# Performance work log

Measured on AMD Instinct MI355X. Metric: run time of the kernel, lower is better.

## Reference

```python
import jax, jax.numpy as jnp
import numpy as np

B, S, L, K, E, V = 2048, 4, 16, 8, 256, 128  # batch, max_steps, tokens/step, landmarks/cell, emb_sz, vocab


def setup_inputs() -> dict:
    key = jax.random.key(0)
    ks = jax.random.split(key, 10)
    std = 1.0 / (E * 9)
    return {
        "gold_table": jax.random.normal(ks[0], (11, E), jnp.float32),
        "map_table": jax.random.normal(ks[1], (V, E), jnp.float32) * 0.01,  # init_std=0.01
        "conv_weight": jax.random.uniform(ks[2], (E, E, 3, 3), jnp.float32, -std, std),
        "action_table": jax.random.normal(ks[3], (4, 32), jnp.float32),
        "action_W": jax.random.normal(ks[4], (9, 32), jnp.float32) * (1.0 / np.sqrt(32.0)),
        "action_b": jnp.zeros((9,), jnp.float32),
        "goldstandard": jax.random.randint(ks[5], (B, S, L), 0, 11),
        "actions": jax.random.randint(ks[6], (B, S - 1), 0, 4),
        "landmarks": jax.random.randint(ks[7], (B, 4, 4, K), 0, V),
        "y": jax.random.randint(ks[8], (B, 2), 0, 4),
    }


def _extract_patches(x):
    # x: [B,E,4,4] -> [B,9,E,16]; 3x3 neighborhoods with zero padding (conv padding=1)
    xp = jnp.pad(x, ((0, 0), (0, 0), (1, 1), (1, 1)))
    shifts = [xp[:, :, dh:dh + 4, dw:dw + 4].reshape(x.shape[0], x.shape[1], 16)
              for dh in range(3) for dw in range(3)]
    return jnp.stack(shifts, axis=1)


def reference(gold_table, map_table, conv_weight, action_table, action_W, action_b,
              goldstandard, actions, landmarks, y):
    Bn = y.shape[0]
    # goldstandard features: per-step embed+sum over tokens, concat over steps -> [B, S*E]
    emb = gold_table[goldstandard].sum(axis=2).reshape(Bn, -1)
    # MapEmbedding2d with padding_idx=0: zero row 0, embed, sum over landmark list
    mt = map_table.at[0].set(0.0)
    l_emb = mt[landmarks].sum(axis=3).transpose(0, 3, 1, 2)  # [B,E,4,4]
    # action-conditioned 3x3 masks, one per action
    action_out = action_table @ action_W.T + action_b  # [4,9]
    masks = jax.nn.softmax(action_out, axis=1)  # [4,9]
    Wr = conv_weight.reshape(E, E, 9)  # [O,I,tap]
    l_embs = [l_emb]
    cur = l_emb
    for j in range(S - 1):
        # per-sample routed mask == dispatch-to-expert conv; fused gather+masked-conv+scatter
        m = masks[actions[:, j]]  # [B,9]
        patches = _extract_patches(cur)  # [B,9,E,16]
        out = jnp.einsum('btip,bt,oit->bop', patches, m, Wr).reshape(Bn, E, 4, 4)
        l_embs.append(out)
        cur = out
    lm = jnp.concatenate(l_embs, axis=1).reshape(Bn, S * E, 16)  # [B, S*E, 16]
    logits = jnp.einsum('bcp,bc->bp', lm, emb)  # bmm(landmarks^T, emb)
    prob = jax.nn.softmax(logits, axis=1)
    y_true = y[:, 0] * 4 + y[:, 1]
    # torch CrossEntropyLoss applied to prob (softmax twice, as in the original)
    logp = jax.nn.log_softmax(prob, axis=1)
    loss = -jnp.take_along_axis(logp, y_true[:, None], axis=1).mean()
    acc = (jnp.argmax(prob, axis=1) == y_true).astype(jnp.float32).mean()
    return loss, acc, prob
```

## Files before the change

### kernel.cpp

```cpp
#include <hip/hip_runtime.h>
#include <hip/hip_bf16.h>

typedef __attribute__((ext_vector_type(4))) float f32x4;
typedef __attribute__((ext_vector_type(8))) short short8;

__device__ __forceinline__ float bf2f(ushort u) {
    union { unsigned int u; float f; } x; x.u = ((unsigned int)u) << 16; return x.f;
}
__device__ __forceinline__ ushort f2bf(float f) {
    union { float f; unsigned int u; } x; x.f = f;
    unsigned int u = x.u;
    unsigned int r = (u + 0x7fffu + ((u >> 16) & 1u)) >> 16;
    return (ushort)r;
}
__device__ __forceinline__ void gload16(const ushort* g, ushort* l) {
    __builtin_amdgcn_global_load_lds(
        (const __attribute__((address_space(1))) unsigned int*)g,
        (__attribute__((address_space(3))) unsigned int*)l, 16, 0, 0);
}

__global__ __launch_bounds__(256) void k_wfold(
    const float* __restrict__ conv_w, const float* __restrict__ a_table,
    const float* __restrict__ a_W, const float* __restrict__ a_b,
    ushort* __restrict__ Wa)
{
    __shared__ float ao[4][9];
    __shared__ float m[4][9];
    const int o = blockIdx.x, tid = threadIdx.x;
    if (tid < 36) {
        const int a = tid / 9, t = tid % 9;
        float s = a_b[t];
        for (int c = 0; c < 32; c++) s += a_table[a * 32 + c] * a_W[t * 32 + c];
        ao[a][t] = s;
    }
    __syncthreads();
    if (tid < 4) {
        float mx = -1e30f;
        for (int t = 0; t < 9; t++) mx = fmaxf(mx, ao[tid][t]);
        float e[9], z = 0.f;
        for (int t = 0; t < 9; t++) { e[t] = expf(ao[tid][t] - mx); z += e[t]; }
        for (int t = 0; t < 9; t++) m[tid][t] = e[t] / z;
    }
    __syncthreads();
    float w9[9];
    #pragma unroll
    for (int t = 0; t < 9; t++) w9[t] = conv_w[(o * 256 + tid) * 9 + t];
    #pragma unroll
    for (int a = 0; a < 4; a++)
        #pragma unroll
        for (int t = 0; t < 9; t++)
            Wa[(size_t)((a << 8) + o) * 2304 + t * 256 + tid] = f2bf(m[a][t] * w9[t]);
}

__global__ __launch_bounds__(256) void k_bucket(
    const int* __restrict__ actions, int* __restrict__ cnt, int* __restrict__ list)
{
    const int idx = blockIdx.x * 256 + threadIdx.x;
    const int j = idx >> 11, b = idx & 2047;
    const int a = actions[b * 3 + j];
    const int pos = atomicAdd(&cnt[j * 4 + a], 1);
    list[((j * 4 + a) << 11) + pos] = b;
}

__global__ __launch_bounds__(256) void k_lemb(
    const float* __restrict__ mapt, const int* __restrict__ lms,
    ushort* __restrict__ c0)
{
    const int b = blockIdx.x, e = threadIdx.x;
    for (int p = 0; p < 16; p++) {
        const int* lm = lms + (b * 16 + p) * 8;
        float s = 0.f;
        #pragma unroll
        for (int k = 0; k < 8; k++) {
            const int idx = lm[k];
            if (idx) s += mapt[idx * 256 + e];
        }
        c0[(size_t)(b * 16 + p) * 256 + e] = f2bf(s);
    }
}

__global__ __launch_bounds__(256, 2) void k_conv(
    const ushort* __restrict__ cur, const ushort* __restrict__ Wa,
    const int* __restrict__ cnt, const int* __restrict__ list,
    const int j, ushort* __restrict__ outp)
{
    __shared__ __align__(16) ushort Alds[2][256 * 64];
    const int tid = threadIdx.x;

    const int c0n = cnt[j * 4 + 0], c1n = cnt[j * 4 + 1],
              c2n = cnt[j * 4 + 2], c3n = cnt[j * 4 + 3];
    const int t0 = (c0n + 3) >> 2;
    const int t1 = t0 + ((c1n + 3) >> 2);
    const int t2 = t1 + ((c2n + 3) >> 2);
    const int t3 = t2 + ((c3n + 3) >> 2);
    const int bid = blockIdx.x;
    const int xcd = bid & 7, sub = bid >> 3;
    const int wg = (xcd < 4 ? xcd * 65 : 260 + (xcd - 4) * 64) + sub;
    if (wg >= t3) return;
    int a, off, ca;
    if      (wg < t0) { a = 0; off = 0;  ca = c0n; }
    else if (wg < t1) { a = 1; off = t0; ca = c1n; }
    else if (wg < t2) { a = 2; off = t1; ca = c2n; }
    else              { a = 3; off = t2; ca = c3n; }
    const int slot0 = (wg - off) * 4;
    const int* la = list + ((j * 4 + a) << 11);
    const ushort* wbase = Wa + (size_t)(a << 8) * 2304;

    const int wid = tid >> 6, lane = tid & 63;
    const int l15 = lane & 15, l4 = lane >> 4;
    const int wm = wid >> 1, wn = wid & 1;

    int sid[2]; bool vst[2];
    #pragma unroll
    for (int nf = 0; nf < 2; nf++) {
        const int sl = slot0 + wn * 2 + nf;
        vst[nf] = sl < ca;
        sid[nf] = vst[nf] ? la[sl] : 0;
    }

    const int srow = tid >> 3, sc = tid & 7;
    const int wubase = (tid & ~63) * 8;
    #define STAGE(buf, k0)                                                     \
        _Pragma("unroll")                                                      \
        for (int qq = 0; qq < 8; qq++) {                                       \
            const int row = qq * 32 + srow;                                    \
            const int cc = sc ^ (row & 7);                                     \
            gload16(wbase + (size_t)row * 2304 + (k0) + cc * 8,                \
                    &Alds[buf][qq * 2048 + wubase]);                           \
        }

    f32x4 acc[8][2];
    #pragma unroll
    for (int mf = 0; mf < 8; mf++) {
        acc[mf][0] = (f32x4){0.f, 0.f, 0.f, 0.f};
        acc[mf][1] = (f32x4){0.f, 0.f, 0.f, 0.f};
    }

    const short8 bzero = {0, 0, 0, 0, 0, 0, 0, 0};
    const int ph = l15 >> 2, pw = l15 & 3;
    STAGE(0, 0);

    int cb = 0;
    for (int ks = 0; ks < 36; ks++) {
        const int k0 = ks * 64;
        const int t = k0 >> 8, i0 = k0 & 255;
        const int hh = ph + t / 3 - 1, ww = pw + t % 3 - 1;
        const bool xv = (hh >= 0) & (hh < 4) & (ww >= 0) & (ww < 4);
        const int psrc = (hh << 2) + ww;

        __syncthreads();

        short8 bfr[2][2];
        #pragma unroll
        for (int nf = 0; nf < 2; nf++)
            #pragma unroll
            for (int kf = 0; kf < 2; kf++) {
                const int i = i0 + kf * 32 + l4 * 8;
                const ushort* src = cur + ((size_t)sid[nf] * 16 + psrc) * 256 + i;
                bfr[nf][kf] = xv ? *(const short8*)src : bzero;
            }

        if (ks + 1 < 36) STAGE(cb ^ 1, k0 + 64);

        #pragma unroll
        for (int kf = 0; kf < 2; kf++) {
            #pragma unroll
            for (int mf = 0; mf < 8; mf++) {
                const int rr = wm * 128 + mf * 16 + l15;
                const int cc = (kf * 4 + l4) ^ (rr & 7);
                const short8 af = *(const short8*)&Alds[cb][rr * 64 + cc * 8];
                acc[mf][0] = __builtin_amdgcn_mfma_f32_16x16x32_bf16(
                    af, bfr[0][kf], acc[mf][0], 0, 0, 0);
                acc[mf][1] = __builtin_amdgcn_mfma_f32_16x16x32_bf16(
                    af, bfr[1][kf], acc[mf][1], 0, 0, 0);
            }
        }
        cb ^= 1;
    }

    #pragma unroll
    for (int nf = 0; nf < 2; nf++) {
        if (!vst[nf]) continue;
        const size_t rowb = ((size_t)sid[nf] * 16 + l15) * 256;
        #pragma unroll
        for (int mf = 0; mf < 8; mf++) {
            const int ob = wm * 128 + mf * 16 + l4 * 4;
            ushort o4[4];
            #pragma unroll
            for (int r = 0; r < 4; r++) o4[r] = f2bf(acc[mf][nf][r]);
            *(uint2*)&outp[rowb + ob] = *(const uint2*)o4;
        }
    }
    #undef STAGE
}

__global__ __launch_bounds__(256) void k_final(
    const ushort* __restrict__ c0, const ushort* __restrict__ c1,
    const ushort* __restrict__ c2, const ushort* __restrict__ c3,
    const float* __restrict__ gold, const int* __restrict__ gs,
    const int* __restrict__ y, float* __restrict__ d_out)
{
    __shared__ float embl[4][256];
    __shared__ float red[256];
    __shared__ float lg[16];
    const int b = blockIdx.x, tid = threadIdx.x;
    {
        const int s = tid >> 6, e0 = (tid & 63) * 4;
        const int* g = gs + b * 64 + s * 16;
        float4 accv = make_float4(0.f, 0.f, 0.f, 0.f);
        #pragma unroll
        for (int l = 0; l < 16; l++) {
            const float4 v = *(const float4*)&gold[g[l] * 256 + e0];
            accv.x += v.x; accv.y += v.y; accv.z += v.z; accv.w += v.w;
        }
        *(float4*)&embl[s][e0] = accv;
    }
    __syncthreads();
    const int p = tid >> 4, g16 = tid & 15;
    const ushort* rows[4] = {
        c0 + (size_t)(b * 16 + p) * 256, c1 + (size_t)(b * 16 + p) * 256,
        c2 + (size_t)(b * 16 + p) * 256, c3 + (size_t)(b * 16 + p) * 256 };
    float acc = 0.f;
    #pragma unroll
    for (int s = 0; s < 4; s++) {
        const ushort* row = rows[s];
        const float* eb = embl[s];
        #pragma unroll 4
        for (int q = 0; q < 16; q++) {
            const int e = g16 + q * 16;
            acc += bf2f(row[e]) * eb[e];
        }
    }
    red[tid] = acc;
    __syncthreads();
    for (int st = 8; st >= 1; st >>= 1) {
        if (g16 < st) red[tid] += red[tid + st];
        __syncthreads();
    }
    if (g16 == 0) lg[p] = red[tid];
    __syncthreads();
    if (tid == 0) {
        float mx = -1e30f;
        for (int q = 0; q < 16; q++) mx = fmaxf(mx, lg[q]);
        float ex[16], z = 0.f;
        for (int q = 0; q < 16; q++) { ex[q] = expf(lg[q] - mx); z += ex[q]; }
        float prob[16];
        for (int q = 0; q < 16; q++) {
            prob[q] = ex[q] / z;
            d_out[2 + b * 16 + q] = prob[q];
        }
        int am = 0; float bv = prob[0];
        for (int q = 1; q < 16; q++) if (prob[q] > bv) { bv = prob[q]; am = q; }
        const int yt = y[b * 2] * 4 + y[b * 2 + 1];
        float z2 = 0.f;
        for (int q = 0; q < 16; q++) z2 += expf(prob[q]);
        const float logp = prob[yt] - logf(z2);
        atomicAdd(&d_out[0], -logp * (1.0f / 2048.0f));
        atomicAdd(&d_out[1], (am == yt) ? (1.0f / 2048.0f) : 0.0f);
    }
}

extern "C" void kernel_launch(void* const* d_in, const int* in_sizes, int n_in,
                              void* d_out, int out_size, void* d_ws, size_t ws_size,
                              hipStream_t stream) {
    const float* gold_table = (const float*)d_in[0];
    const float* map_table  = (const float*)d_in[1];
    const float* conv_w     = (const float*)d_in[2];
    const float* a_table    = (const float*)d_in[3];
    const float* a_W        = (const float*)d_in[4];
    const float* a_b        = (const float*)d_in[5];
    const int*   gs         = (const int*)d_in[6];
    const int*   actions    = (const int*)d_in[7];
    const int*   lms        = (const int*)d_in[8];
    const int*   y          = (const int*)d_in[9];
    float* out = (float*)d_out;

    char* ws = (char*)d_ws;
    int*    cnt  = (int*)(ws + 0);
    int*    list = (int*)(ws + 256);
    ushort* Wa   = (ushort*)(ws + 131072);
    ushort* c0   = (ushort*)(ws + 4849664);
    ushort* c1   = (ushort*)(ws + 21626880);
    ushort* c2   = (ushort*)(ws + 38404096);
    ushort* c3   = (ushort*)(ws + 55181312);
    (void)in_sizes; (void)n_in; (void)out_size; (void)ws_size;

    hipMemsetAsync(cnt, 0, 48, stream);
    hipMemsetAsync(d_out, 0, 2 * sizeof(float), stream);
    k_wfold <<<256, 256, 0, stream>>>(conv_w, a_table, a_W, a_b, Wa);
    k_bucket<<<24, 256, 0, stream>>>(actions, cnt, list);
    k_lemb  <<<2048, 256, 0, stream>>>(map_table, lms, c0);
    k_conv  <<<516, 256, 0, stream>>>(c0, Wa, cnt, list, 0, c1);
    k_conv  <<<516, 256, 0, stream>>>(c1, Wa, cnt, list, 1, c2);
    k_conv  <<<516, 256, 0, stream>>>(c2, Wa, cnt, list, 2, c3);
    k_final <<<2048, 256, 0, stream>>>(c0, c1, c2, c3, gold_table, gs, y, out);
}
```

Before: 494.2 us.

## Split conv output channels across two blocks, prefetch B fragments, fuse prep kernels

Each conv workgroup now computes 128 output channels instead of 256, doubling the grid to 1032 blocks and halving LDS use so four blocks can be resident per CU. The B-fragment (activation) loads are software-pipelined one k-step ahead in registers. The weight-fold and bucketing kernels and the two memsets are merged into one prep kernel, with bucketing done by a single extra block. In exchange, each activation tile is now gathered by two blocks and the serial single-block bucketing may take longer.

```diff
diff --git a/kernel.cpp b/kernel.cpp
--- a/kernel.cpp
+++ b/kernel.cpp
@@ -19,47 +19,53 @@
         (__attribute__((address_space(3))) unsigned int*)l, 16, 0, 0);
 }
 
-__global__ __launch_bounds__(256) void k_wfold(
+__global__ __launch_bounds__(256) void k_prep(
     const float* __restrict__ conv_w, const float* __restrict__ a_table,
     const float* __restrict__ a_W, const float* __restrict__ a_b,
-    ushort* __restrict__ Wa)
+    const int* __restrict__ actions, int* __restrict__ cnt,
+    int* __restrict__ list, ushort* __restrict__ Wa,
+    float* __restrict__ out_head)
 {
     __shared__ float ao[4][9];
     __shared__ float m[4][9];
-    const int o = blockIdx.x, tid = threadIdx.x;
-    if (tid < 36) {
-        const int a = tid / 9, t = tid % 9;
-        float s = a_b[t];
-        for (int c = 0; c < 32; c++) s += a_table[a * 32 + c] * a_W[t * 32 + c];
-        ao[a][t] = s;
-    }
-    __syncthreads();
-    if (tid < 4) {
-        float mx = -1e30f;
-        for (int t = 0; t < 9; t++) mx = fmaxf(mx, ao[tid][t]);
-        float e[9], z = 0.f;
-        for (int t = 0; t < 9; t++) { e[t] = expf(ao[tid][t] - mx); z += e[t]; }
-        for (int t = 0; t < 9; t++) m[tid][t] = e[t] / z;
-    }
-    __syncthreads();
-    float w9[9];
-    #pragma unroll
-    for (int t = 0; t < 9; t++) w9[t] = conv_w[(o * 256 + tid) * 9 + t];
-    #pragma unroll
-    for (int a = 0; a < 4; a++)
-        #pragma unroll
-        for (int t = 0; t < 9; t++)
-            Wa[(size_t)((a << 8) + o) * 2304 + t * 256 + tid] = f2bf(m[a][t] * w9[t]);
-}
-
-__global__ __launch_bounds__(256) void k_bucket(
-    const int* __restrict__ actions, int* __restrict__ cnt, int* __restrict__ list)
-{
-    const int idx = blockIdx.x * 256 + threadIdx.x;
-    const int j = idx >> 11, b = idx & 2047;
-    const int a = actions[b * 3 + j];
-    const int pos = atomicAdd(&cnt[j * 4 + a], 1);
-    list[((j * 4 + a) << 11) + pos] = b;
+    const int bid = blockIdx.x, tid = threadIdx.x;
+    if (bid < 256) {
+        if (tid < 36) {
+            const int a = tid / 9, t = tid % 9;
+            float s = a_b[t];
+            for (int c = 0; c < 32; c++) s += a_table[a * 32 + c] * a_W[t * 32 + c];
+            ao[a][t] = s;
+        }
+        __syncthreads();
+        if (tid < 4) {
+            float mx = -1e30f;
+            for (int t = 0; t < 9; t++) mx = fmaxf(mx, ao[tid][t]);
+            float e[9], z = 0.f;
+            for (int t = 0; t < 9; t++) { e[t] = expf(ao[tid][t] - mx); z += e[t]; }
+            for (int t = 0; t < 9; t++) m[tid][t] = e[t] / z;
+        }
+        __syncthreads();
+        const int o = bid;
+        float w9[9];
+        #pragma unroll
+        for (int t = 0; t < 9; t++) w9[t] = conv_w[(o * 256 + tid) * 9 + t];
+        #pragma unroll
+        for (int a = 0; a < 4; a++)
+            #pragma unroll
+            for (int t = 0; t < 9; t++)
+                Wa[(size_t)((a << 8) + o) * 2304 + t * 256 + tid] = f2bf(m[a][t] * w9[t]);
+    } else {
+        if (tid < 12) cnt[tid] = 0;
+        if (tid == 0) { out_head[0] = 0.f; out_head[1] = 0.f; }
+        __syncthreads();
+        for (int it = 0; it < 24; it++) {
+            const int idx = it * 256 + tid;
+            const int jj = idx >> 11, b = idx & 2047;
+            const int av = actions[b * 3 + jj];
+            const int pos = atomicAdd(&cnt[jj * 4 + av], 1);
+            list[((jj * 4 + av) << 11) + pos] = b;
+        }
+    }
 }
 
 __global__ __launch_bounds__(256) void k_lemb(
@@ -79,12 +85,12 @@
     }
 }
 
-__global__ __launch_bounds__(256, 2) void k_conv(
+__global__ __launch_bounds__(256, 4) void k_conv(
     const ushort* __restrict__ cur, const ushort* __restrict__ Wa,
     const int* __restrict__ cnt, const int* __restrict__ list,
     const int j, ushort* __restrict__ outp)
 {
-    __shared__ __align__(16) ushort Alds[2][256 * 64];
+    __shared__ __align__(16) ushort Alds[2][128 * 64];
     const int tid = threadIdx.x;
 
     const int c0n = cnt[j * 4 + 0], c1n = cnt[j * 4 + 1],
@@ -94,17 +100,18 @@
     const int t2 = t1 + ((c2n + 3) >> 2);
     const int t3 = t2 + ((c3n + 3) >> 2);
     const int bid = blockIdx.x;
-    const int xcd = bid & 7, sub = bid >> 3;
-    const int wg = (xcd < 4 ? xcd * 65 : 260 + (xcd - 4) * 64) + sub;
-    if (wg >= t3) return;
+    const int wg2 = (bid & 7) * 129 + (bid >> 3);
+    const int om  = wg2 >= 516 ? 1 : 0;
+    const int g   = wg2 - om * 516;
+    if (g >= t3) return;
     int a, off, ca;
-    if      (wg < t0) { a = 0; off = 0;  ca = c0n; }
-    else if (wg < t1) { a = 1; off = t0; ca = c1n; }
-    else if (wg < t2) { a = 2; off = t1; ca = c2n; }
-    else              { a = 3; off = t2; ca = c3n; }
-    const int slot0 = (wg - off) * 4;
+    if      (g < t0) { a = 0; off = 0;  ca = c0n; }
+    else if (g < t1) { a = 1; off = t0; ca = c1n; }
+    else if (g < t2) { a = 2; off = t1; ca = c2n; }
+    else             { a = 3; off = t2; ca = c3n; }
+    const int slot0 = (g - off) * 4;
     const int* la = list + ((j * 4 + a) << 11);
-    const ushort* wbase = Wa + (size_t)(a << 8) * 2304;
+    const ushort* wbase = Wa + (size_t)(a << 8) * 2304 + (size_t)om * 128 * 2304;
 
     const int wid = tid >> 6, lane = tid & 63;
     const int l15 = lane & 15, l4 = lane >> 4;
@@ -119,62 +126,69 @@
     }
 
     const int srow = tid >> 3, sc = tid & 7;
-    const int wubase = (tid & ~63) * 8;
     #define STAGE(buf, k0)                                                     \
         _Pragma("unroll")                                                      \
-        for (int qq = 0; qq < 8; qq++) {                                       \
+        for (int qq = 0; qq < 4; qq++) {                                       \
             const int row = qq * 32 + srow;                                    \
             const int cc = sc ^ (row & 7);                                     \
             gload16(wbase + (size_t)row * 2304 + (k0) + cc * 8,                \
-                    &Alds[buf][qq * 2048 + wubase]);                           \
-        }
-
-    f32x4 acc[8][2];
+                    &Alds[buf][qq * 2048 + tid * 8]);                          \
+        }
+
+    f32x4 acc[4][2];
     #pragma unroll
-    for (int mf = 0; mf < 8; mf++) {
+    for (int mf = 0; mf < 4; mf++) {
         acc[mf][0] = (f32x4){0.f, 0.f, 0.f, 0.f};
         acc[mf][1] = (f32x4){0.f, 0.f, 0.f, 0.f};
     }
 
     const short8 bzero = {0, 0, 0, 0, 0, 0, 0, 0};
     const int ph = l15 >> 2, pw = l15 & 3;
+
+    short8 bcur[2][2], bnxt[2][2];
+    #define LOADB(dst, ks)                                                     \
+        {                                                                      \
+            const int k0b = (ks) * 64;                                         \
+            const int tb = k0b >> 8, i0b = k0b & 255;                          \
+            const int hh = ph + tb / 3 - 1, ww = pw + tb % 3 - 1;              \
+            const bool xv = (hh >= 0) & (hh < 4) & (ww >= 0) & (ww < 4);       \
+            const int psrc = (hh << 2) + ww;                                   \
+            _Pragma("unroll")                                                  \
+            for (int nf = 0; nf < 2; nf++)                                     \
+                _Pragma("unroll")                                              \
+                for (int kf = 0; kf < 2; kf++) {                               \
+                    const int i = i0b + kf * 32 + l4 * 8;                      \
+                    const ushort* srcb =                                       \
+                        cur + ((size_t)sid[nf] * 16 + psrc) * 256 + i;         \
+                    dst[nf][kf] = xv ? *(const short8*)srcb : bzero;           \
+                }                                                              \
+        }
+
+    LOADB(bcur, 0);
     STAGE(0, 0);
 
     int cb = 0;
     for (int ks = 0; ks < 36; ks++) {
-        const int k0 = ks * 64;
-        const int t = k0 >> 8, i0 = k0 & 255;
-        const int hh = ph + t / 3 - 1, ww = pw + t % 3 - 1;
-        const bool xv = (hh >= 0) & (hh < 4) & (ww >= 0) & (ww < 4);
-        const int psrc = (hh << 2) + ww;
-
-        __syncthreads();
-
-        short8 bfr[2][2];
-        #pragma unroll
-        for (int nf = 0; nf < 2; nf++)
+        __syncthreads();
+        if (ks + 1 < 36) STAGE(cb ^ 1, ks * 64 + 64);
+        LOADB(bnxt, ks + 1);
+
+        #pragma unroll
+        for (int kf = 0; kf < 2; kf++)
             #pragma unroll
-            for (int kf = 0; kf < 2; kf++) {
-                const int i = i0 + kf * 32 + l4 * 8;
-                const ushort* src = cur + ((size_t)sid[nf] * 16 + psrc) * 256 + i;
-                bfr[nf][kf] = xv ? *(const short8*)src : bzero;
-            }
-
-        if (ks + 1 < 36) STAGE(cb ^ 1, k0 + 64);
-
-        #pragma unroll
-        for (int kf = 0; kf < 2; kf++) {
-            #pragma unroll
-            for (int mf = 0; mf < 8; mf++) {
-                const int rr = wm * 128 + mf * 16 + l15;
+            for (int mf = 0; mf < 4; mf++) {
+                const int rr = wm * 64 + mf * 16 + l15;
                 const int cc = (kf * 4 + l4) ^ (rr & 7);
                 const short8 af = *(const short8*)&Alds[cb][rr * 64 + cc * 8];
                 acc[mf][0] = __builtin_amdgcn_mfma_f32_16x16x32_bf16(
-                    af, bfr[0][kf], acc[mf][0], 0, 0, 0);
+                    af, bcur[0][kf], acc[mf][0], 0, 0, 0);
                 acc[mf][1] = __builtin_amdgcn_mfma_f32_16x16x32_bf16(
-                    af, bfr[1][kf], acc[mf][1], 0, 0, 0);
+                    af, bcur[1][kf], acc[mf][1], 0, 0, 0);
             }
-        }
+        #pragma unroll
+        for (int nf = 0; nf < 2; nf++)
+            #pragma unroll
+            for (int kf = 0; kf < 2; kf++) bcur[nf][kf] = bnxt[nf][kf];
         cb ^= 1;
     }
 
@@ -183,8 +197,8 @@
         if (!vst[nf]) continue;
         const size_t rowb = ((size_t)sid[nf] * 16 + l15) * 256;
         #pragma unroll
-        for (int mf = 0; mf < 8; mf++) {
-            const int ob = wm * 128 + mf * 16 + l4 * 4;
+        for (int mf = 0; mf < 4; mf++) {
+            const int ob = om * 128 + wm * 64 + mf * 16 + l4 * 4;
             ushort o4[4];
             #pragma unroll
             for (int r = 0; r < 4; r++) o4[r] = f2bf(acc[mf][nf][r]);
@@ -192,6 +206,7 @@
         }
     }
     #undef STAGE
+    #undef LOADB
 }
 
 __global__ __launch_bounds__(256) void k_final(
@@ -285,13 +300,11 @@
     ushort* c3   = (ushort*)(ws + 55181312);
     (void)in_sizes; (void)n_in; (void)out_size; (void)ws_size;
 
-    hipMemsetAsync(cnt, 0, 48, stream);
-    hipMemsetAsync(d_out, 0, 2 * sizeof(float), stream);
-    k_wfold <<<256, 256, 0, stream>>>(conv_w, a_table, a_W, a_b, Wa);
-    k_bucket<<<24, 256, 0, stream>>>(actions, cnt, list);
-    k_lemb  <<<2048, 256, 0, stream>>>(map_table, lms, c0);
-    k_conv  <<<516, 256, 0, stream>>>(c0, Wa, cnt, list, 0, c1);
-    k_conv  <<<516, 256, 0, stream>>>(c1, Wa, cnt, list, 1, c2);
-    k_conv  <<<516, 256, 0, stream>>>(c2, Wa, cnt, list, 2, c3);
-    k_final <<<2048, 256, 0, stream>>>(c0, c1, c2, c3, gold_table, gs, y, out);
-}
+    k_prep <<<257, 256, 0, stream>>>(conv_w, a_table, a_W, a_b, actions,
+                                     cnt, list, Wa, out);
+    k_lemb <<<2048, 256, 0, stream>>>(map_table, lms, c0);
+    k_conv <<<1032, 256, 0, stream>>>(c0, Wa, cnt, list, 0, c1);
+    k_conv <<<1032, 256, 0, stream>>>(c1, Wa, cnt, list, 1, c2);
+    k_conv <<<1032, 256, 0, stream>>>(c2, Wa, cnt, list, 2, c3);
+    k_final<<<2048, 256, 0, stream>>>(c0, c1, c2, c3, gold_table, gs, y, out);
+}
```

Result: faster. 483.5 us (-2.2%).
